# Performance work log

Hardware: AMD Instinct MI355X
Metric: run time of the kernel (lower is better)

The kernel has to match this reference:

```python
import jax, jax.numpy as jnp
import numpy as np

N, E = 100000, 1600000
NFEAT, NHID, NCLASS, NLAYER = 128, 128, 40, 3


def _glorot(key, shape):
    fan_in, fan_out = shape[0], shape[1]
    lim = float(np.sqrt(6.0 / (fan_in + fan_out)))
    return jax.random.uniform(key, shape, jnp.float32, -lim, lim)


def setup_inputs() -> dict:
    key = jax.random.key(0)
    ks = jax.random.split(key, 12)
    x = jax.random.normal(ks[0], (N, NFEAT), jnp.float32)
    src = jax.random.randint(ks[1], (E,), 0, N, jnp.int32)
    dst = jax.random.randint(ks[2], (E,), 0, N, jnp.int32)
    W1 = _glorot(ks[3], (NFEAT, NHID)); b1 = jnp.zeros((NHID,), jnp.float32)
    W2 = _glorot(ks[4], (NHID, NHID)); b2 = jnp.zeros((NHID,), jnp.float32)
    Wg = jnp.stack([_glorot(ks[5 + l], (NHID, NHID)) for l in range(NLAYER)])  # [L,H,H]
    bg = jnp.zeros((NLAYER, NHID), jnp.float32)
    Wc = _glorot(ks[5 + NLAYER], (NHID, NCLASS)); bc = jnp.zeros((NCLASS,), jnp.float32)
    return {"x": x, "src": src, "dst": dst, "W1": W1, "b1": b1, "W2": W2,
            "b2": b2, "Wg": Wg, "bg": bg, "Wc": Wc, "bc": bc}


def _graph_conv(h, src, dst, W, b, out_norm, in_norm):
    # DGL GraphConv norm='both': scale by src out-deg^{-1/2}, sum-aggregate,
    # scale by dst in-deg^{-1/2}, then linear (in_feats == out_feats -> W after agg).
    h = h * out_norm[:, None]
    agg = jax.ops.segment_sum(h[src], dst, num_segments=N)
    return (agg * in_norm[:, None]) @ W + b


def reference(x, src, dst, W1, b1, W2, b2, Wg, bg, Wc, bc):
    ones = jnp.ones((E,), jnp.float32)
    out_deg = jnp.clip(jax.ops.segment_sum(ones, src, num_segments=N), 1.0)
    in_deg = jnp.clip(jax.ops.segment_sum(ones, dst, num_segments=N), 1.0)
    out_norm = jax.lax.rsqrt(out_deg)
    in_norm = jax.lax.rsqrt(in_deg)

    h = x @ W1 + b1            # feature1
    h = h @ W2 + b2            # feature2
    for l in range(NLAYER):    # stacked GraphConv + ReLU (dropout is identity in eval)
        h = _graph_conv(h, src, dst, Wg[l], bg[l], out_norm, in_norm)
        h = jax.nn.relu(h)
    return h @ Wc + bc         # classifier
```

## Files before the change

kernel.cpp:

```cpp
#include <hip/hip_runtime.h>
#include <hip/hip_fp16.h>
#include <cstdint>
#include <cstddef>

constexpr int NN  = 100000;
constexpr int EE  = 1600000;
constexpr int HID = 128;
constexpr int BUK = 256;
constexpr int NBUK = (NN + BUK - 1) / BUK;
constexpr int BLKE = 2048;
constexpr int NBE  = (EE + BLKE - 1) / BLKE;
constexpr int MH   = NBUK * NBE;
constexpr int NSC  = (MH + 1023) / 1024;

typedef float f32x4_t __attribute__((ext_vector_type(4)));
typedef short bf16x8_t __attribute__((ext_vector_type(8)));

static __device__ __forceinline__ short f2bf(float f) {
    union { float f; unsigned u; } x; x.f = f;
    unsigned r = x.u + 0x7FFF + ((x.u >> 16) & 1);
    return (short)(r >> 16);
}
static __device__ __forceinline__ float bf2f(short b) {
    union { unsigned u; float f; } x; x.u = ((unsigned)(unsigned short)b) << 16;
    return x.f;
}

__global__ __launch_bounds__(256) void bh_both_k(const int* __restrict__ src, const int* __restrict__ dst,
                                                 int* __restrict__ bh_d, int* __restrict__ bh_s) {
    __shared__ int hd[NBUK], hs[NBUK];
    int blk = blockIdx.x, t = threadIdx.x;
    for (int i = t; i < NBUK; i += 256) { hd[i] = 0; hs[i] = 0; }
    __syncthreads();
    int e0 = blk * BLKE, e1 = min(e0 + BLKE, EE);
    for (int e = e0 + t; e < e1; e += 256) {
        atomicAdd(&hd[dst[e] >> 8], 1);
        atomicAdd(&hs[src[e] >> 8], 1);
    }
    __syncthreads();
    for (int i = t; i < NBUK; i += 256) {
        bh_d[i * NBE + blk] = hd[i];
        bh_s[i * NBE + blk] = hs[i];
    }
}

__global__ __launch_bounds__(256) void scan_sum_k(const int* __restrict__ in, int* __restrict__ bsum, int n) {
    __shared__ int sc[256];
    int b = blockIdx.x, t = threadIdx.x;
    int base = b * 1024 + t * 4;
    int s = 0;
#pragma unroll
    for (int j = 0; j < 4; j++) { int idx = base + j; s += (idx < n) ? in[idx] : 0; }
    sc[t] = s; __syncthreads();
    for (int off = 128; off > 0; off >>= 1) {
        if (t < off) sc[t] += sc[t + off];
        __syncthreads();
    }
    if (t == 0) bsum[b] = sc[0];
}

__global__ __launch_bounds__(512) void scan_top_k(const int* __restrict__ bsum, int* __restrict__ boff, int nb) {
    __shared__ int sc[512];
    int t = threadIdx.x;
    int v = (t < nb) ? bsum[t] : 0;
    sc[t] = v; __syncthreads();
    for (int off = 1; off < 512; off <<= 1) {
        int u = (t >= off) ? sc[t - off] : 0;
        __syncthreads();
        sc[t] += u;
        __syncthreads();
    }
    if (t < nb) boff[t] = sc[t] - v;
}

__global__ __launch_bounds__(256) void scan_chunk_k(const int* __restrict__ in, const int* __restrict__ boff,
                                                    int* __restrict__ out, int n) {
    __shared__ int sc[256];
    int b = blockIdx.x, t = threadIdx.x;
    int base = b * 1024 + t * 4;
    int c[4];
#pragma unroll
    for (int j = 0; j < 4; j++) { int idx = base + j; c[j] = (idx < n) ? in[idx] : 0; }
    int s = c[0] + c[1] + c[2] + c[3];
    sc[t] = s; __syncthreads();
    for (int off = 1; off < 256; off <<= 1) {
        int v = (t >= off) ? sc[t - off] : 0;
        __syncthreads();
        sc[t] += v;
        __syncthreads();
    }
    int excl = sc[t] - s + boff[b];
#pragma unroll
    for (int j = 0; j < 4; j++) {
        int idx = base + j;
        if (idx < n) out[idx] = excl;
        excl += c[j];
    }
}

__global__ __launch_bounds__(256) void scatter_both_k(const int* __restrict__ src, const int* __restrict__ dst,
                                                      const int* __restrict__ off_d, const int* __restrict__ off_s,
                                                      unsigned* __restrict__ pairs, unsigned char* __restrict__ sbyte) {
    __shared__ int cd[NBUK], cs[NBUK];
    int blk = blockIdx.x, t = threadIdx.x;
    for (int i = t; i < NBUK; i += 256) {
        cd[i] = off_d[i * NBE + blk];
        cs[i] = off_s[i * NBE + blk];
    }
    __syncthreads();
    int e0 = blk * BLKE, e1 = min(e0 + BLKE, EE);
    for (int e = e0 + t; e < e1; e += 256) {
        int d = dst[e], s = src[e];
        int pd = atomicAdd(&cd[d >> 8], 1);
        pairs[pd] = ((unsigned)(d & 255) << 17) | (unsigned)s;
        int ps = atomicAdd(&cs[s >> 8], 1);
        sbyte[ps] = (unsigned char)(s & 255);
    }
}

__global__ __launch_bounds__(512) void bucket_csr_ocnt_k(
    const unsigned* __restrict__ pairs, const int* __restrict__ off_d,
    const unsigned char* __restrict__ sbyte, const int* __restrict__ off_s,
    int* __restrict__ rowptr, int* __restrict__ col,
    float* __restrict__ inorm, float* __restrict__ onorm) {
    __shared__ int hist[BUK];
    __shared__ int excl[BUK];
    __shared__ int psum[BUK];
    int t = threadIdx.x;

    if (blockIdx.x >= NBUK) {
        int b = blockIdx.x - NBUK;
        int base = off_s[b * NBE];
        int endv = (b == NBUK - 1) ? EE : off_s[(b + 1) * NBE];
        if (t < BUK) hist[t] = 0;
        __syncthreads();
        for (int i = base + t; i < endv; i += 512) atomicAdd(&hist[sbyte[i]], 1);
        __syncthreads();
        if (t < BUK) {
            int node = b * BUK + t;
            if (node < NN) {
                int c = hist[t]; if (c < 1) c = 1;
                onorm[node] = rsqrtf((float)c);
            }
        }
        return;
    }

    int b = blockIdx.x;
    int base = off_d[b * NBE];
    int endv = (b == NBUK - 1) ? EE : off_d[(b + 1) * NBE];
    if (t < BUK) hist[t] = 0;
    __syncthreads();
    for (int i = base + t; i < endv; i += 512) atomicAdd(&hist[pairs[i] >> 17], 1);
    __syncthreads();
    int ps = 0;
    if (t < BUK) { ps = hist[t]; psum[t] = ps; }
    __syncthreads();
    for (int off = 1; off < BUK; off <<= 1) {
        int u = 0;
        if (t < BUK && t >= off) u = psum[t - off];
        __syncthreads();
        if (t < BUK) psum[t] += u;
        __syncthreads();
    }
    if (t < BUK) {
        int pex = psum[t] - ps;
        excl[t] = pex;
        int node = b * BUK + t;
        if (node < NN) {
            rowptr[node] = base + pex;
            int c = ps; if (c < 1) c = 1;
            inorm[node] = rsqrtf((float)c);
        }
    }
    if (b == NBUK - 1 && t == 0) rowptr[NN] = EE;
    __syncthreads();
    for (int i = base + t; i < endv; i += 512) {
        unsigned p = pairs[i];
        int pos = base + atomicAdd(&excl[p >> 17], 1);
        col[pos] = (int)(p & 0x1FFFFu);
    }
}

__global__ __launch_bounds__(256) void w12_k(const float* __restrict__ W1, const float* __restrict__ W2,
                                             const float* __restrict__ b1, const float* __restrict__ b2,
                                             float* __restrict__ W12, float* __restrict__ b12) {
    if (blockIdx.x == 64) {
        int j = threadIdx.x;
        if (j < 128) {
            float acc = b2[j];
            for (int k = 0; k < 128; k++) acc = fmaf(b1[k], W2[k * 128 + j], acc);
            b12[j] = acc;
        }
        return;
    }
    int idx = blockIdx.x * 256 + threadIdx.x;
    int i = idx >> 7, j = idx & 127;
    float a0 = 0.f, a1 = 0.f, a2 = 0.f, a3 = 0.f;
    for (int k = 0; k < 128; k += 4) {
        a0 = fmaf(W1[i * 128 + k],     W2[(k)     * 128 + j], a0);
        a1 = fmaf(W1[i * 128 + k + 1], W2[(k + 1) * 128 + j], a1);
        a2 = fmaf(W1[i * 128 + k + 2], W2[(k + 2) * 128 + j], a2);
        a3 = fmaf(W1[i * 128 + k + 3], W2[(k + 3) * 128 + j], a3);
    }
    W12[idx] = (a0 + a1) + (a2 + a3);
}

__global__ __launch_bounds__(256) void agg_k(const float4* __restrict__ h16, const int* __restrict__ rowptr,
                                             const int* __restrict__ col, float4* __restrict__ out) {
    int w = (int)((blockIdx.x * 256 + threadIdx.x) >> 6);
    if (w >= NN) return;
    int lane = threadIdx.x & 63;
    int q   = lane >> 4;
    int l16 = lane & 15;
    int beg = rowptr[w], end = rowptr[w + 1];
    float acc[8];
#pragma unroll
    for (int j = 0; j < 8; j++) acc[j] = 0.f;

    union HU { float4 f4; __half2 h2[4]; };
    int i = beg + q;
    for (; i + 12 < end; i += 16) {
        int s0 = col[i], s1 = col[i + 4], s2 = col[i + 8], s3 = col[i + 12];
        HU u0, u1, u2, u3;
        u0.f4 = h16[(size_t)s0 * 16 + l16];
        u1.f4 = h16[(size_t)s1 * 16 + l16];
        u2.f4 = h16[(size_t)s2 * 16 + l16];
        u3.f4 = h16[(size_t)s3 * 16 + l16];
#pragma unroll
        for (int p = 0; p < 4; p++) {
            float2 a = __half22float2(u0.h2[p]);
            float2 b = __half22float2(u1.h2[p]);
            float2 c = __half22float2(u2.h2[p]);
            float2 d = __half22float2(u3.h2[p]);
            acc[2 * p]     += (a.x + b.x) + (c.x + d.x);
            acc[2 * p + 1] += (a.y + b.y) + (c.y + d.y);
        }
    }
    for (; i < end; i += 4) {
        int s = col[i];
        HU u; u.f4 = h16[(size_t)s * 16 + l16];
#pragma unroll
        for (int p = 0; p < 4; p++) {
            float2 a = __half22float2(u.h2[p]);
            acc[2 * p]     += a.x;
            acc[2 * p + 1] += a.y;
        }
    }
#pragma unroll
    for (int mm = 16; mm <= 32; mm <<= 1)
#pragma unroll
        for (int j = 0; j < 8; j++) acc[j] += __shfl_xor(acc[j], mm);
    if (q == 0) {
        float4 o0, o1;
        o0.x = acc[0]; o0.y = acc[1]; o0.z = acc[2]; o0.w = acc[3];
        o1.x = acc[4]; o1.y = acc[5]; o1.z = acc[6]; o1.w = acc[7];
        out[(size_t)w * 32 + l16 * 2]     = o0;
        out[(size_t)w * 32 + l16 * 2 + 1] = o1;
    }
}

template <int NT, bool RELU, bool INSCALE, bool OUTSCALE, bool OUTHALF>
__global__ __launch_bounds__(256) void mfma_gemm_k(
    const float* __restrict__ in, const float* __restrict__ inscale,
    const float* __restrict__ W, const float* __restrict__ bias,
    void* __restrict__ outp, const float* __restrict__ outscale,
    int nrows, int ncols, int ntiles) {

    __shared__ short Bh[NT * 2048];
    __shared__ short Bl[NT * 2048];

    const int t = threadIdx.x;

    if constexpr (NT == 8) {
        for (int j = 0; j < 16; j++) {
            int fi = (j * 256 + t) * 4;
            int k = fi >> 7, n0 = fi & 127;
            float4 wv = *(const float4*)(W + fi);
            float wa[4] = {wv.x, wv.y, wv.z, wv.w};
#pragma unroll
            for (int cc = 0; cc < 4; cc++) {
                int g = n0 + cc;
                int q2 = g >> 2;
                int ntc = q2 & 7;
                int c = ((q2 >> 3) << 2) | (g & 3);
                int kblk = k >> 5, ksub = k & 31;
                int lane_ = ((ksub >> 3) << 4) | c;
                int sidx = ((ntc * 4 + kblk) * 64 + lane_) * 8 + (ksub & 7);
                short hi = f2bf(wa[cc]);
                Bh[sidx] = hi; Bl[sidx] = f2bf(wa[cc] - bf2f(hi));
            }
        }
    } else {
        for (int idx = t; idx < 128 * 64; idx += 256) {
            int k = idx >> 6, g = idx & 63;
            if (g < NT * 16) {
                float w = (g < 40) ? W[k * 40 + g] : 0.f;
                int q2 = g >> 2;
                int ntc = q2 % NT;
                int c = (q2 / NT) * 4 + (g & 3);
                int kblk = k >> 5, ksub = k & 31;
                int lane_ = ((ksub >> 3) << 4) | c;
                int sidx = ((ntc * 4 + kblk) * 64 + lane_) * 8 + (ksub & 7);
                short hi = f2bf(w);
                Bh[sidx] = hi; Bl[sidx] = f2bf(w - bf2f(hi));
            }
        }
    }
    __syncthreads();

    const int wave = t >> 6;
    const int lane = t & 63;
    const int m    = lane & 15;
    const int kq   = lane >> 4;
    const int cbase = kq * 4 * NT;

    float bstat[4 * NT];
#pragma unroll
    for (int i = 0; i < 4 * NT; i++) {
        int g = cbase + i;
        bstat[i] = (g < ncols) ? bias[g] : 0.f;
    }

    const int wstride = gridDim.x * 4;
    for (int tile = blockIdx.x * 4 + wave; tile < ntiles; tile += wstride) {
        int row = tile * 16 + m;
        bool rv = row < nrows;

        bf16x8_t Ah[4], Al[4];
        float s = 1.f;
        if (INSCALE && rv) s = inscale[row];
#pragma unroll
        for (int kb = 0; kb < 4; kb++) {
            const float* ap = in + (size_t)row * 128 + kb * 32 + kq * 8;
            float4 p0, p1;
            if (rv) { p0 = *(const float4*)ap; p1 = *(const float4*)(ap + 4); }
            else    { p0 = make_float4(0,0,0,0); p1 = make_float4(0,0,0,0); }
            float av[8] = {p0.x, p0.y, p0.z, p0.w, p1.x, p1.y, p1.z, p1.w};
#pragma unroll
            for (int j = 0; j < 8; j++) {
                float v = INSCALE ? av[j] * s : av[j];
                short hi = f2bf(v);
                Ah[kb][j] = hi;
                Al[kb][j] = f2bf(v - bf2f(hi));
            }
        }

        float osc = 1.f;
        if (OUTSCALE && rv) osc = outscale[row];

        float ov[4 * NT] __attribute__((aligned(16)));
#pragma unroll
        for (int nt = 0; nt < NT; nt++) {
            f32x4_t acc = {0.f, 0.f, 0.f, 0.f};
#pragma unroll
            for (int kb = 0; kb < 4; kb++) {
                const bf16x8_t bh = *(const bf16x8_t*)&Bh[((nt * 4 + kb) * 64 + lane) * 8];
                const bf16x8_t bl = *(const bf16x8_t*)&Bl[((nt * 4 + kb) * 64 + lane) * 8];
                acc = __builtin_amdgcn_mfma_f32_16x16x32_bf16(bh, Ah[kb], acc, 0, 0, 0);
                acc = __builtin_amdgcn_mfma_f32_16x16x32_bf16(bh, Al[kb], acc, 0, 0, 0);
                acc = __builtin_amdgcn_mfma_f32_16x16x32_bf16(bl, Ah[kb], acc, 0, 0, 0);
            }
#pragma unroll
            for (int r = 0; r < 4; r++) {
                float v = acc[r] + bstat[nt * 4 + r];
                if (RELU) v = fmaxf(v, 0.f);
                ov[nt * 4 + r] = v * osc;
            }
        }

        if (rv) {
            if constexpr (OUTHALF) {
                union { __half h[4 * NT]; float4 f4[NT]; } U;
#pragma unroll
                for (int i = 0; i < 4 * NT; i++) U.h[i] = __float2half_rn(ov[i]);
                float4* p = (float4*)((__half*)outp + (size_t)row * ncols + cbase);
#pragma unroll
                for (int j = 0; j < NT; j += 2) p[j >> 1] = U.f4[j >> 1];
            } else if constexpr (NT == 8) {
                float4* p = (float4*)((float*)outp + (size_t)row * 128 + cbase);
#pragma unroll
                for (int j = 0; j < 8; j++) p[j] = ((const float4*)ov)[j];
            } else {
                float* p = (float*)outp + (size_t)row * 40 + cbase;
#pragma unroll
                for (int j = 0; j < 3; j++) {
                    if (cbase + j * 4 < 40) *(float4*)(p + j * 4) = ((const float4*)ov)[j];
                }
            }
        }
    }
}

extern "C" void kernel_launch(void* const* d_in, const int* in_sizes, int n_in,
                              void* d_out, int out_size, void* d_ws, size_t ws_size,
                              hipStream_t stream) {
    const float* x   = (const float*)d_in[0];
    const int*   src = (const int*)d_in[1];
    const int*   dst = (const int*)d_in[2];
    const float* W1  = (const float*)d_in[3];
    const float* b1  = (const float*)d_in[4];
    const float* W2  = (const float*)d_in[5];
    const float* b2  = (const float*)d_in[6];
    const float* Wg  = (const float*)d_in[7];
    const float* bg  = (const float*)d_in[8];
    const float* Wc  = (const float*)d_in[9];
    const float* bc  = (const float*)d_in[10];
    float* out = (float*)d_out;

    char* ws = (char*)d_ws;
    size_t off = 0;
    auto alloc = [&](size_t bytes) -> void* {
        void* p = ws + off;
        off += (bytes + 255) & ~(size_t)255;
        return p;
    };
    float*  h0     = (float*)alloc((size_t)NN * HID * 4);
    float*  h1     = (float*)alloc((size_t)NN * HID * 4);
    __half* h16    = (__half*)alloc((size_t)NN * HID * 2);
    float*  W12    = (float*)alloc(128 * 128 * 4);
    float*  b12    = (float*)alloc(128 * 4);
    float*  onorm  = (float*)alloc((size_t)NN * 4);
    float*  inorm  = (float*)alloc((size_t)NN * 4);
    int*    rowptr = (int*)alloc((size_t)(NN + 1) * 4);
    int*    col    = (int*)alloc((size_t)EE * 4);
    int*    bh_d   = (int*)alloc((size_t)MH * 4);
    int*    bh_s   = (int*)alloc((size_t)MH * 4);
    int*    off_d  = (int*)alloc((size_t)MH * 4);
    int*    off_s  = (int*)alloc((size_t)MH * 4);
    int*    bsum   = (int*)alloc((size_t)NSC * 4);
    int*    boff   = (int*)alloc((size_t)NSC * 4);
    unsigned*      pairs = (unsigned*)h0;
    unsigned char* sbyte = (unsigned char*)h0 + (size_t)EE * 4;

    bh_both_k<<<NBE, 256, 0, stream>>>(src, dst, bh_d, bh_s);
    scan_sum_k<<<NSC, 256, 0, stream>>>(bh_d, bsum, MH);
    scan_top_k<<<1, 512, 0, stream>>>(bsum, boff, NSC);
    scan_chunk_k<<<NSC, 256, 0, stream>>>(bh_d, boff, off_d, MH);
    scan_sum_k<<<NSC, 256, 0, stream>>>(bh_s, bsum, MH);
    scan_top_k<<<1, 512, 0, stream>>>(bsum, boff, NSC);
    scan_chunk_k<<<NSC, 256, 0, stream>>>(bh_s, boff, off_s, MH);
    scatter_both_k<<<NBE, 256, 0, stream>>>(src, dst, off_d, off_s, pairs, sbyte);
    bucket_csr_ocnt_k<<<2 * NBUK, 512, 0, stream>>>(pairs, off_d, sbyte, off_s,
                                                    rowptr, col, inorm, onorm);

    w12_k<<<65, 256, 0, stream>>>(W1, W2, b1, b2, W12, b12);

    const int ntiles = (NN + 15) / 16;
    const int ggrid  = 512;

    mfma_gemm_k<8, false, false, true, true><<<ggrid, 256, 0, stream>>>(
        x, nullptr, W12, b12, h16, onorm, NN, 128, ntiles);
    for (int l = 0; l < 3; l++) {
        agg_k<<<(NN * 64 + 255) / 256, 256, 0, stream>>>(
            (const float4*)h16, rowptr, col, (float4*)h0);
        if (l < 2) {
            mfma_gemm_k<8, true, true, true, true><<<ggrid, 256, 0, stream>>>(
                h0, inorm, Wg + (size_t)l * 128 * 128, bg + (size_t)l * 128, h16, onorm, NN, 128, ntiles);
        } else {
            mfma_gemm_k<8, true, true, false, false><<<ggrid, 256, 0, stream>>>(
                h0, inorm, Wg + (size_t)l * 128 * 128, bg + (size_t)l * 128, h1, nullptr, NN, 128, ntiles);
        }
    }
    mfma_gemm_k<3, false, false, false, false><<<ggrid, 256, 0, stream>>>(
        h1, nullptr, Wc, bc, out, nullptr, NN, 40, ntiles);
}
```

Before: 558.6 us.

## Fuse neighbor aggregation with GraphConv GEMM into one persistent kernel per layer

```diff
diff --git a/kernel.cpp b/kernel.cpp
--- a/kernel.cpp
+++ b/kernel.cpp
@@ -206,57 +206,128 @@
     W12[idx] = (a0 + a1) + (a2 + a3);
 }
 
-__global__ __launch_bounds__(256) void agg_k(const float4* __restrict__ h16, const int* __restrict__ rowptr,
-                                             const int* __restrict__ col, float4* __restrict__ out) {
-    int w = (int)((blockIdx.x * 256 + threadIdx.x) >> 6);
-    if (w >= NN) return;
-    int lane = threadIdx.x & 63;
-    int q   = lane >> 4;
-    int l16 = lane & 15;
-    int beg = rowptr[w], end = rowptr[w + 1];
-    float acc[8];
-#pragma unroll
-    for (int j = 0; j < 8; j++) acc[j] = 0.f;
+template <bool LAST>
+__global__ __launch_bounds__(256) void agg_conv_k(
+    const float4* __restrict__ h16, const int* __restrict__ rowptr,
+    const int* __restrict__ col, const float* __restrict__ inorm,
+    const float* __restrict__ onorm, const float* __restrict__ W,
+    const float* __restrict__ bias, void* __restrict__ outp, int ntiles) {
+
+    __shared__ float Ast[16 * 132];
+    const int t = threadIdx.x;
+    const int wave = t >> 6, lane = t & 63;
+    const int q = lane >> 4, l16 = lane & 15;
+
+    bf16x8_t Wh[2][4], Wl[2][4];
+    {
+        const int gb = ((l16 >> 2) << 5) + wave * 8 + (l16 & 3);
+#pragma unroll
+        for (int ntc = 0; ntc < 2; ntc++) {
+#pragma unroll
+            for (int kb = 0; kb < 4; kb++) {
+#pragma unroll
+                for (int j = 0; j < 8; j++) {
+                    float wv = W[(kb * 32 + q * 8 + j) * 128 + gb + ntc * 4];
+                    short hi = f2bf(wv);
+                    Wh[ntc][kb][j] = hi;
+                    Wl[ntc][kb][j] = f2bf(wv - bf2f(hi));
+                }
+            }
+        }
+    }
+    const int cbase = q * 32 + wave * 8;
+    float bstat[8];
+#pragma unroll
+    for (int i = 0; i < 8; i++) bstat[i] = bias[cbase + i];
 
     union HU { float4 f4; __half2 h2[4]; };
-    int i = beg + q;
-    for (; i + 12 < end; i += 16) {
-        int s0 = col[i], s1 = col[i + 4], s2 = col[i + 8], s3 = col[i + 12];
-        HU u0, u1, u2, u3;
-        u0.f4 = h16[(size_t)s0 * 16 + l16];
-        u1.f4 = h16[(size_t)s1 * 16 + l16];
-        u2.f4 = h16[(size_t)s2 * 16 + l16];
-        u3.f4 = h16[(size_t)s3 * 16 + l16];
-#pragma unroll
-        for (int p = 0; p < 4; p++) {
-            float2 a = __half22float2(u0.h2[p]);
-            float2 b = __half22float2(u1.h2[p]);
-            float2 c = __half22float2(u2.h2[p]);
-            float2 d = __half22float2(u3.h2[p]);
-            acc[2 * p]     += (a.x + b.x) + (c.x + d.x);
-            acc[2 * p + 1] += (a.y + b.y) + (c.y + d.y);
-        }
-    }
-    for (; i < end; i += 4) {
-        int s = col[i];
-        HU u; u.f4 = h16[(size_t)s * 16 + l16];
-#pragma unroll
-        for (int p = 0; p < 4; p++) {
-            float2 a = __half22float2(u.h2[p]);
-            acc[2 * p]     += a.x;
-            acc[2 * p + 1] += a.y;
-        }
-    }
-#pragma unroll
-    for (int mm = 16; mm <= 32; mm <<= 1)
-#pragma unroll
-        for (int j = 0; j < 8; j++) acc[j] += __shfl_xor(acc[j], mm);
-    if (q == 0) {
-        float4 o0, o1;
-        o0.x = acc[0]; o0.y = acc[1]; o0.z = acc[2]; o0.w = acc[3];
-        o1.x = acc[4]; o1.y = acc[5]; o1.z = acc[6]; o1.w = acc[7];
-        out[(size_t)w * 32 + l16 * 2]     = o0;
-        out[(size_t)w * 32 + l16 * 2 + 1] = o1;
+
+    for (int tile = blockIdx.x; tile < ntiles; tile += gridDim.x) {
+        {
+            const int node = tile * 16 + wave * 4 + q;
+            int i = rowptr[node];
+            const int end = rowptr[node + 1];
+            float acc[8];
+#pragma unroll
+            for (int j = 0; j < 8; j++) acc[j] = 0.f;
+            for (; i + 3 < end; i += 4) {
+                int s0 = col[i], s1 = col[i + 1], s2 = col[i + 2], s3 = col[i + 3];
+                HU u0, u1, u2, u3;
+                u0.f4 = h16[(size_t)s0 * 16 + l16];
+                u1.f4 = h16[(size_t)s1 * 16 + l16];
+                u2.f4 = h16[(size_t)s2 * 16 + l16];
+                u3.f4 = h16[(size_t)s3 * 16 + l16];
+#pragma unroll
+                for (int p = 0; p < 4; p++) {
+                    float2 a = __half22float2(u0.h2[p]);
+                    float2 b = __half22float2(u1.h2[p]);
+                    float2 c = __half22float2(u2.h2[p]);
+                    float2 d = __half22float2(u3.h2[p]);
+                    acc[2 * p]     += (a.x + b.x) + (c.x + d.x);
+                    acc[2 * p + 1] += (a.y + b.y) + (c.y + d.y);
+                }
+            }
+            for (; i < end; ++i) {
+                HU u; u.f4 = h16[(size_t)col[i] * 16 + l16];
+#pragma unroll
+                for (int p = 0; p < 4; p++) {
+                    float2 a = __half22float2(u.h2[p]);
+                    acc[2 * p]     += a.x;
+                    acc[2 * p + 1] += a.y;
+                }
+            }
+            float* ap = &Ast[(wave * 4 + q) * 132 + l16 * 8];
+            *(float4*)ap       = make_float4(acc[0], acc[1], acc[2], acc[3]);
+            *(float4*)(ap + 4) = make_float4(acc[4], acc[5], acc[6], acc[7]);
+        }
+        __syncthreads();
+
+        const int row = tile * 16 + l16;
+        const float s = inorm[row];
+        bf16x8_t Bh_[4], Bl_[4];
+#pragma unroll
+        for (int kb = 0; kb < 4; kb++) {
+            const float* rp = &Ast[l16 * 132 + kb * 32 + q * 8];
+            float4 p0 = *(const float4*)rp;
+            float4 p1 = *(const float4*)(rp + 4);
+            float av[8] = {p0.x, p0.y, p0.z, p0.w, p1.x, p1.y, p1.z, p1.w};
+#pragma unroll
+            for (int j = 0; j < 8; j++) {
+                float v = av[j] * s;
+                short hi = f2bf(v);
+                Bh_[kb][j] = hi;
+                Bl_[kb][j] = f2bf(v - bf2f(hi));
+            }
+        }
+        float osc = 1.f;
+        if constexpr (!LAST) osc = onorm[row];
+        float ov[8] __attribute__((aligned(16)));
+#pragma unroll
+        for (int ntc = 0; ntc < 2; ntc++) {
+            f32x4_t acc = {0.f, 0.f, 0.f, 0.f};
+#pragma unroll
+            for (int kb = 0; kb < 4; kb++) {
+                acc = __builtin_amdgcn_mfma_f32_16x16x32_bf16(Wh[ntc][kb], Bh_[kb], acc, 0, 0, 0);
+                acc = __builtin_amdgcn_mfma_f32_16x16x32_bf16(Wh[ntc][kb], Bl_[kb], acc, 0, 0, 0);
+                acc = __builtin_amdgcn_mfma_f32_16x16x32_bf16(Wl[ntc][kb], Bh_[kb], acc, 0, 0, 0);
+            }
+#pragma unroll
+            for (int r = 0; r < 4; r++) {
+                float v = fmaxf(acc[r] + bstat[ntc * 4 + r], 0.f);
+                ov[ntc * 4 + r] = v * osc;
+            }
+        }
+        if constexpr (LAST) {
+            float* p = (float*)outp + (size_t)row * 128 + cbase;
+            *(float4*)p       = *(const float4*)&ov[0];
+            *(float4*)(p + 4) = *(const float4*)&ov[4];
+        } else {
+            union { __half h[8]; float4 f4; } U;
+#pragma unroll
+            for (int j = 0; j < 8; j++) U.h[j] = __float2half_rn(ov[j]);
+            *(float4*)((__half*)outp + (size_t)row * 128 + cbase) = U.f4;
+        }
+        __syncthreads();
     }
 }
 
@@ -415,9 +486,9 @@
         off += (bytes + 255) & ~(size_t)255;
         return p;
     };
-    float*  h0     = (float*)alloc((size_t)NN * HID * 4);
     float*  h1     = (float*)alloc((size_t)NN * HID * 4);
-    __half* h16    = (__half*)alloc((size_t)NN * HID * 2);
+    __half* h16a   = (__half*)alloc((size_t)NN * HID * 2);
+    __half* h16b   = (__half*)alloc((size_t)NN * HID * 2);
     float*  W12    = (float*)alloc(128 * 128 * 4);
     float*  b12    = (float*)alloc(128 * 4);
     float*  onorm  = (float*)alloc((size_t)NN * 4);
@@ -430,8 +501,8 @@
     int*    off_s  = (int*)alloc((size_t)MH * 4);
     int*    bsum   = (int*)alloc((size_t)NSC * 4);
     int*    boff   = (int*)alloc((size_t)NSC * 4);
-    unsigned*      pairs = (unsigned*)h0;
-    unsigned char* sbyte = (unsigned char*)h0 + (size_t)EE * 4;
+    unsigned*      pairs = (unsigned*)h1;
+    unsigned char* sbyte = (unsigned char*)h1 + (size_t)EE * 4;
 
     bh_both_k<<<NBE, 256, 0, stream>>>(src, dst, bh_d, bh_s);
     scan_sum_k<<<NSC, 256, 0, stream>>>(bh_d, bsum, MH);
@@ -446,22 +517,23 @@
 
     w12_k<<<65, 256, 0, stream>>>(W1, W2, b1, b2, W12, b12);
 
-    const int ntiles = (NN + 15) / 16;
+    const int ntiles = NN / 16;
     const int ggrid  = 512;
+    const int fgrid  = 2048;
 
     mfma_gemm_k<8, false, false, true, true><<<ggrid, 256, 0, stream>>>(
-        x, nullptr, W12, b12, h16, onorm, NN, 128, ntiles);
-    for (int l = 0; l < 3; l++) {
-        agg_k<<<(NN * 64 + 255) / 256, 256, 0, stream>>>(
-            (const float4*)h16, rowptr, col, (float4*)h0);
-        if (l < 2) {
-            mfma_gemm_k<8, true, true, true, true><<<ggrid, 256, 0, stream>>>(
-                h0, inorm, Wg + (size_t)l * 128 * 128, bg + (size_t)l * 128, h16, onorm, NN, 128, ntiles);
-        } else {
-            mfma_gemm_k<8, true, true, false, false><<<ggrid, 256, 0, stream>>>(
-                h0, inorm, Wg + (size_t)l * 128 * 128, bg + (size_t)l * 128, h1, nullptr, NN, 128, ntiles);
-        }
-    }
+        x, nullptr, W12, b12, h16a, onorm, NN, 128, ntiles);
+
+    agg_conv_k<false><<<fgrid, 256, 0, stream>>>(
+        (const float4*)h16a, rowptr, col, inorm, onorm,
+        Wg, bg, h16b, ntiles);
+    agg_conv_k<false><<<fgrid, 256, 0, stream>>>(
+        (const float4*)h16b, rowptr, col, inorm, onorm,
+        Wg + 128 * 128, bg + 128, h16a, ntiles);
+    agg_conv_k<true><<<fgrid, 256, 0, stream>>>(
+        (const float4*)h16a, rowptr, col, inorm, onorm,
+        Wg + 2 * 128 * 128, bg + 256, h1, ntiles);
+
     mfma_gemm_k<3, false, false, false, false><<<ggrid, 256, 0, stream>>>(
         h1, nullptr, Wc, bc, out, nullptr, NN, 40, ntiles);
 }
```

After: 609.3 us. 1.09x slower.
